# Optimization experiments

Measured on AMD Instinct MI355X. Metric: run time of the kernel, lower is better.

The kernel has to match this reference:

```python
import jax, jax.numpy as jnp
import numpy as np

B, L, DIM, HEADS = 2, 2048, 1536, 12
HD = DIM // HEADS  # 128
C = HD // 2        # 64 rotary pairs
EPS = 1e-6


def setup_inputs() -> dict:
    key = jax.random.key(0)
    ks = jax.random.split(key, 8)
    x = jax.random.normal(ks[0], (B, L, DIM), jnp.float32)
    # ragged grids: sample0 fills L, sample1 has 2*24*32 = 1536 valid tokens
    grid_sizes = jnp.array([[2, 32, 32], [2, 24, 32]], dtype=jnp.int32)
    seq_lens = jnp.array([2048, 1536], dtype=jnp.int32)
    # rope freqs table [1024, C] (cos/sin of pos * inv_freq)
    pos = jnp.arange(1024, dtype=jnp.float32)[:, None]
    inv = 1.0 / (10000.0 ** (jnp.arange(C, dtype=jnp.float32) / C))
    ang = pos * inv
    freqs_cos, freqs_sin = jnp.cos(ang), jnp.sin(ang)
    init = lambda k: jax.random.normal(k, (DIM, DIM), jnp.float32) / np.sqrt(DIM)
    return dict(
        x=x, seq_lens=seq_lens, grid_sizes=grid_sizes,
        freqs_cos=freqs_cos, freqs_sin=freqs_sin,
        Wq=init(ks[1]), bq=jnp.zeros((DIM,), jnp.float32),
        Wk=init(ks[2]), bk=jnp.zeros((DIM,), jnp.float32),
        Wv=init(ks[3]), bv=jnp.zeros((DIM,), jnp.float32),
        Wo=init(ks[4]), bo=jnp.zeros((DIM,), jnp.float32),
        gq=jnp.ones((DIM,), jnp.float32), gk=jnp.ones((DIM,), jnp.float32),
    )


def _rope_one(xb, grid, cos, sin):
    # xb: [L, n, d]; grid: (f, h, w); cos/sin: [1024, C]
    f, h, w = grid[0], grid[1], grid[2]
    c = cos.shape[1]
    c2 = c // 3
    c1 = c - 2 * c2  # freqs split [c1, c2, c2] over axes (f, h, w)
    p = jnp.arange(xb.shape[0])
    hw = h * w
    valid = p < f * hw
    fi = jnp.where(valid, p // hw, 0)
    hi = jnp.where(valid, (p // w) % h, 0)
    wi = jnp.where(valid, p % w, 0)
    cos_p = jnp.concatenate([cos[fi, :c1], cos[hi, c1:c1 + c2], cos[wi, c1 + c2:]], axis=-1)
    sin_p = jnp.concatenate([sin[fi, :c1], sin[hi, c1:c1 + c2], sin[wi, c1 + c2:]], axis=-1)
    # positions beyond seq_len pass through unrotated (identity rotation)
    cos_p = jnp.where(valid[:, None], cos_p, 1.0)[:, None, :]  # [L,1,C]
    sin_p = jnp.where(valid[:, None], sin_p, 0.0)[:, None, :]
    xr, xi = xb[..., 0::2], xb[..., 1::2]
    out_r = xr * cos_p - xi * sin_p
    out_i = xr * sin_p + xi * cos_p
    return jnp.stack([out_r, out_i], axis=-1).reshape(xb.shape)


_rope_apply = jax.vmap(_rope_one, in_axes=(0, 0, None, None))


def _rms(t, g):
    t32 = t.astype(jnp.float32)
    return (t32 * jax.lax.rsqrt(jnp.mean(t32 * t32, axis=-1, keepdims=True) + EPS) * g).astype(t.dtype)


def reference(x, seq_lens, grid_sizes, freqs_cos, freqs_sin,
              Wq, bq, Wk, bk, Wv, bv, Wo, bo, gq, gk):
    b, s = x.shape[:2]
    n, d = HEADS, HD
    q = _rms(x @ Wq + bq, gq).reshape(b, s, n, d)
    k = _rms(x @ Wk + bk, gk).reshape(b, s, n, d)
    v = (x @ Wv + bv).reshape(b, s, n, d)
    q = _rope_apply(q, grid_sizes, freqs_cos, freqs_sin)
    k = _rope_apply(k, grid_sizes, freqs_cos, freqs_sin)
    scale = 1.0 / np.sqrt(d).astype(np.float32)
    scores = jnp.einsum('bqnd,bknd->bnqk', q, k) * scale
    kmask = jnp.arange(s)[None, :] < seq_lens[:, None]  # [b, s] key validity
    scores = jnp.where(kmask[:, None, None, :], scores, jnp.float32(-1e9))
    attn = jax.nn.softmax(scores, axis=-1)
    out = jnp.einsum('bnqk,bknd->bqnd', attn, v).reshape(b, s, n * d)
    return out @ Wo + bo
```

## Files before the change

kernel.cpp:

```cpp
#include <hip/hip_runtime.h>
#include <hip/hip_bf16.h>

#define DIM   1536
#define HEADS 12
#define HD    128
#define LSEQ  2048
#define NB    2
#define NTOK  (NB*LSEQ)

using f32x4  = __attribute__((ext_vector_type(4))) float;
using f32x16 = __attribute__((ext_vector_type(16))) float;
using s16x8  = __attribute__((ext_vector_type(8))) short;
using u16x4  = __attribute__((ext_vector_type(4))) unsigned short;

__device__ __forceinline__ unsigned short f2bf(float f) {
  unsigned int u = __builtin_bit_cast(unsigned int, f);
  u += 0x7fffu + ((u >> 16) & 1u);
  return (unsigned short)(u >> 16);
}
__device__ __forceinline__ float bf2f(unsigned short u) {
  return __builtin_bit_cast(float, (unsigned int)u << 16);
}
__device__ __forceinline__ unsigned pk2(float a, float b) {
  unsigned r;
  asm("v_cvt_pk_bf16_f32 %0, %1, %2" : "=v"(r) : "v"(a), "v"(b));
  return r;
}
__device__ __forceinline__ unsigned long long pack4bf(float a, float b, float c, float d) {
  return (unsigned long long)f2bf(a) | ((unsigned long long)f2bf(b) << 16) |
         ((unsigned long long)f2bf(c) << 32) | ((unsigned long long)f2bf(d) << 48);
}
__device__ __forceinline__ void plswap(unsigned &x, unsigned &y) {
  asm volatile("v_permlane32_swap_b32 %0, %1" : "+v"(x), "+v"(y));
}
__device__ __forceinline__ void gload_lds16(const void* g, void* l) {
  __builtin_amdgcn_global_load_lds(
      (__attribute__((address_space(1))) void*)const_cast<void*>(g),
      (__attribute__((address_space(3))) void*)l,
      16, 0, 0);
}

__global__ __launch_bounds__(256) void cvt_x(const float* __restrict__ x,
                                             unsigned short* __restrict__ xb, int n) {
  int i = (blockIdx.x * 256 + threadIdx.x) * 4;
  int stride = gridDim.x * 256 * 4;
  for (; i < n; i += stride) {
    f32x4 v = *(const f32x4*)(x + i);
    u16x4 o;
    o[0] = f2bf(v[0]); o[1] = f2bf(v[1]); o[2] = f2bf(v[2]); o[3] = f2bf(v[3]);
    *(u16x4*)(xb + i) = o;
  }
}

__global__ __launch_bounds__(256) void wtrans(const float* W0, const float* W1,
                                              const float* W2, const float* W3,
                                              unsigned short* __restrict__ Wt) {
  const float* W = blockIdx.z == 0 ? W0 : blockIdx.z == 1 ? W1 : blockIdx.z == 2 ? W2 : W3;
  unsigned short* out = Wt + (size_t)blockIdx.z * DIM * DIM;
  const int n0 = blockIdx.x * 64, k0 = blockIdx.y * 64;
  __shared__ unsigned short t[64][68];
  const int tid = threadIdx.x;
#pragma unroll
  for (int i = 0; i < 16; i++) {
    int idx = tid + i * 256;
    int r = idx >> 6, c = idx & 63;
    t[r][c] = f2bf(W[(size_t)(k0 + r) * DIM + n0 + c]);
  }
  __syncthreads();
#pragma unroll
  for (int i = 0; i < 16; i++) {
    int idx = tid + i * 256;
    int r = idx >> 6, c = idx & 63;
    out[(size_t)(n0 + r) * DIM + k0 + c] = t[c][r];
  }
}

__global__ __launch_bounds__(256) void gemm_bt(
    const unsigned short* __restrict__ A, const unsigned short* __restrict__ Bt,
    void* __restrict__ Cv,
    const float* __restrict__ b0, const float* __restrict__ b1, const float* __restrict__ b2,
    int M, int N, int K, int biasMode, int outBf16) {
  __shared__ __align__(16) unsigned short As[128 * 64];
  __shared__ __align__(16) unsigned short Bs[128 * 64];
  const int tid = threadIdx.x;
  const int lane = tid & 63, w = tid >> 6;
  const int wr = w >> 1, wc = w & 1;
  const int l15 = lane & 15, g4 = lane >> 4;
  const int nwg = gridDim.x * gridDim.y;
  const int bidf = blockIdx.y * gridDim.x + blockIdx.x;
  const int cpx = nwg >> 3;
  const int sw = (bidf & 7) * cpx + (bidf >> 3);
  const int m0 = (sw / gridDim.x) * 128, n0 = (sw % gridDim.x) * 128;

  f32x4 acc[4][4];
#pragma unroll
  for (int i = 0; i < 4; i++)
#pragma unroll
    for (int j = 0; j < 4; j++) acc[i][j] = (f32x4){0.f, 0.f, 0.f, 0.f};

  for (int kt = 0; kt < K; kt += 64) {
    __syncthreads();
#pragma unroll
    for (int i = 0; i < 4; i++) {
      int c = tid + i * 256;
      int row = c >> 3, g = c & 7;
      int gs = g ^ (row & 7);
      gload_lds16(A + (size_t)(m0 + row) * K + kt + gs * 8, As + c * 8);
    }
#pragma unroll
    for (int i = 0; i < 4; i++) {
      int c = tid + i * 256;
      int row = c >> 3, g = c & 7;
      int gs = g ^ (row & 7);
      gload_lds16(Bt + (size_t)(n0 + row) * K + kt + gs * 8, Bs + c * 8);
    }
    __syncthreads();
#pragma unroll
    for (int kk = 0; kk < 2; kk++) {
      s16x8 af[4], bfr[4];
#pragma unroll
      for (int m = 0; m < 4; m++) {
        int row = wr * 64 + m * 16 + l15;
        int off = row * 128 + ((kk * 64 + g4 * 16) ^ ((row & 7) << 4));
        af[m] = *(const s16x8*)((const char*)As + off);
      }
#pragma unroll
      for (int n = 0; n < 4; n++) {
        int row = wc * 64 + n * 16 + l15;
        int off = row * 128 + ((kk * 64 + g4 * 16) ^ ((row & 7) << 4));
        bfr[n] = *(const s16x8*)((const char*)Bs + off);
      }
#pragma unroll
      for (int m = 0; m < 4; m++)
#pragma unroll
        for (int n = 0; n < 4; n++)
          acc[m][n] = __builtin_amdgcn_mfma_f32_16x16x32_bf16(af[m], bfr[n], acc[m][n], 0, 0, 0);
    }
  }
#pragma unroll
  for (int m = 0; m < 4; m++)
#pragma unroll
    for (int n = 0; n < 4; n++)
#pragma unroll
      for (int r = 0; r < 4; r++) {
        int grow = m0 + wr * 64 + m * 16 + g4 * 4 + r;
        int gcol = n0 + wc * 64 + n * 16 + l15;
        float bias = (biasMode == 1)
                         ? b0[gcol]
                         : (gcol < 1536 ? b0[gcol]
                                        : (gcol < 3072 ? b1[gcol - 1536] : b2[gcol - 3072]));
        float val = acc[m][n][r] + bias;
        if (outBf16) ((unsigned short*)Cv)[(size_t)grow * N + gcol] = f2bf(val);
        else         ((float*)Cv)[(size_t)grow * N + gcol] = val;
      }
}

__global__ __launch_bounds__(256) void rmsrope(
    const unsigned short* __restrict__ qkvb,
    const float* __restrict__ gq, const float* __restrict__ gk,
    const int* __restrict__ grid_sizes,
    const float* __restrict__ fcos, const float* __restrict__ fsin,
    unsigned short* __restrict__ qb, unsigned short* __restrict__ kb) {
  const int t = blockIdx.x;
  const int b = t >> 11, l = t & 2047;
  const int tid = threadIdx.x;
  __shared__ float qrow[1536], krow[1536];
  __shared__ float red[8];
  const unsigned short* rq = qkvb + (size_t)t * 4608;
  const unsigned short* rk = rq + 1536;
  float sq = 0.f, sk = 0.f;
  if (tid < 192) {
    s16x8 vq = *(const s16x8*)(rq + tid * 8);
    s16x8 vk = *(const s16x8*)(rk + tid * 8);
#pragma unroll
    for (int j = 0; j < 8; j++) {
      float a = bf2f((unsigned short)vq[j]); qrow[tid * 8 + j] = a; sq += a * a;
      float c = bf2f((unsigned short)vk[j]); krow[tid * 8 + j] = c; sk += c * c;
    }
  }
  for (int o = 32; o; o >>= 1) { sq += __shfl_down(sq, o); sk += __shfl_down(sk, o); }
  if ((tid & 63) == 0) { red[tid >> 6] = sq; red[4 + (tid >> 6)] = sk; }
  __syncthreads();
  const float rsq = rsqrtf((red[0] + red[1] + red[2] + red[3]) * (1.f / 1536.f) + 1e-6f);
  const float rsk = rsqrtf((red[4] + red[5] + red[6] + red[7]) * (1.f / 1536.f) + 1e-6f);
  const float QS = 0.08838834764831845f * 1.4426950408889634f;
  const int fg = grid_sizes[b * 3 + 0], hg = grid_sizes[b * 3 + 1], wg = grid_sizes[b * 3 + 2];
  const int hw = hg * wg;
  const bool valid = l < fg * hw;
  const int fi = valid ? l / hw : 0;
  const int hi = valid ? (l / wg) % hg : 0;
  const int wi = valid ? l % wg : 0;
  const size_t obase = (((size_t)b * HEADS) * LSEQ + l) * HD;
  for (int i = tid; i < HEADS * 64; i += 256) {
    int hd = i >> 6, j = i & 63;
    float c, s;
    if (valid) {
      int idx = j < 22 ? fi : (j < 43 ? hi : wi);
      c = fcos[idx * 64 + j]; s = fsin[idx * 64 + j];
    } else { c = 1.f; s = 0.f; }
    int col = hd * 128 + 2 * j;
    size_t o = obase + (size_t)hd * LSEQ * HD + 2 * j;
    float xr = qrow[col] * rsq * gq[col];
    float xi = qrow[col + 1] * rsq * gq[col + 1];
    float q0 = (xr * c - xi * s) * QS, q1 = (xr * s + xi * c) * QS;
    *(unsigned int*)(qb + o) = (unsigned int)f2bf(q0) | ((unsigned int)f2bf(q1) << 16);
    xr = krow[col] * rsk * gk[col];
    xi = krow[col + 1] * rsk * gk[col + 1];
    *(unsigned int*)(kb + o) =
        (unsigned int)f2bf(xr * c - xi * s) | ((unsigned int)f2bf(xr * s + xi * c) << 16);
  }
}

__global__ __launch_bounds__(256) void vtrans(const unsigned short* __restrict__ qkvb,
                                              unsigned short* __restrict__ vt) {
  const int lt = blockIdx.x, h = blockIdx.y, b = blockIdx.z;
  const int l0 = lt * 64;
  __shared__ unsigned short tile[64][130];
  const int tid = threadIdx.x;
#pragma unroll
  for (int i = 0; i < 4; i++) {
    int idx = tid + i * 256;
    int tk = idx >> 4, dc = (idx & 15) * 8;
    s16x8 v = *(const s16x8*)(qkvb + (size_t)(b * 2048 + l0 + tk) * 4608 + 3072 + h * 128 + dc);
#pragma unroll
    for (int j = 0; j < 8; j++) tile[tk][dc + j] = (unsigned short)v[j];
  }
  __syncthreads();
  const size_t ob = (((size_t)b * HEADS + h) * HD) * LSEQ + l0;
#pragma unroll
  for (int i = 0; i < 4; i++) {
    int idx = tid + i * 256;
    int d = idx >> 3, ck = (idx & 7) * 8;
    s16x8 o;
#pragma unroll
    for (int j = 0; j < 8; j++) o[j] = (short)tile[ck + j][d];
    *(s16x8*)(vt + ob + (size_t)d * LSEQ + ck) = o;
  }
}

__global__ __launch_bounds__(128) void flash(
    const unsigned short* __restrict__ qb, const unsigned short* __restrict__ kb,
    const unsigned short* __restrict__ vt, const int* __restrict__ seq_lens,
    unsigned short* __restrict__ ob) {
  const int orig = blockIdx.x + 32 * (blockIdx.y + 12 * blockIdx.z);
  const int wg = (orig & 7) * 96 + (orig >> 3);
  const int qt = wg & 31;
  const int hb = wg >> 5;
  const int hh = hb % 12, b = hb / 12;
  const int tid = threadIdx.x, lane = tid & 63, w = tid >> 6;
  const int l31 = lane & 31, hi = lane >> 5;
  __shared__ __align__(16) unsigned short Ks[2][32 * 128];
  __shared__ __align__(16) unsigned short Vs[2][128 * 32];
  const size_t bh = (size_t)b * HEADS + hh;
  const int q0 = qt * 64 + w * 32;

  s16x8 qf[8];
  {
    const unsigned short* qp = qb + (bh * LSEQ + q0 + l31) * HD + hi * 8;
#pragma unroll
    for (int s = 0; s < 8; s++) qf[s] = *(const s16x8*)(qp + s * 16);
  }
  const int ntile = seq_lens[b] >> 5;
  asm volatile("s_waitcnt vmcnt(0)" ::: "memory");

  f32x16 acc[4];
#pragma unroll
  for (int d = 0; d < 4; d++)
#pragma unroll
    for (int r = 0; r < 16; r++) acc[d][r] = 0.f;
  float mrow = -1e30f, ls = 0.f;

#define STAGE_K(T, BUF)                                                                \
  _Pragma("unroll") for (int i = 0; i < 4; i++) {                                      \
    int c = tid + i * 128, row = c >> 4, seg = c & 15, ss = seg ^ (row & 15);          \
    gload_lds16(kb + (bh * LSEQ + (T) * 32 + row) * HD + ss * 8, &Ks[BUF][0] + c * 8); \
  }
#define STAGE_V(T, BUF)                                                                \
  _Pragma("unroll") for (int i = 0; i < 4; i++) {                                      \
    int c = tid + i * 128, row = c >> 2, seg = c & 3, ss = seg ^ ((row >> 1) & 3);     \
    gload_lds16(vt + (bh * HD + row) * LSEQ + (T) * 32 + ss * 8, &Vs[BUF][0] + c * 8); \
  }

  STAGE_K(0, 0); STAGE_V(0, 0);
  STAGE_K(1, 1); STAGE_V(1, 1);

  for (int kt = 0; kt < ntile; kt++) {
    const int cur = kt & 1;
    asm volatile("s_waitcnt vmcnt(8)" ::: "memory");
    __builtin_amdgcn_s_barrier();
    __builtin_amdgcn_sched_barrier(0);
    f32x16 st0;
#pragma unroll
    for (int r = 0; r < 16; r++) st0[r] = 0.f;
    const char* ksb = (const char*)&Ks[cur][0];
    __builtin_amdgcn_s_setprio(1);
#pragma unroll
    for (int s = 0; s < 8; s++) {
      int g = 2 * s + hi;
      s16x8 kf = *(const s16x8*)(ksb + l31 * 256 + ((g ^ (l31 & 15)) << 4));
      st0 = __builtin_amdgcn_mfma_f32_32x32x16_bf16(kf, qf[s], st0, 0, 0, 0);
    }
    __builtin_amdgcn_s_setprio(0);
    f32x16 mt;
#pragma unroll
    for (int r = 0; r < 16; r++) mt[r] = st0[r];
#pragma unroll
    for (int off = 8; off; off >>= 1)
#pragma unroll
      for (int r = 0; r < off; r++) mt[r] = fmaxf(mt[r], mt[r + off]);
    float mx = fmaxf(mt[0], __shfl_xor(mt[0], 32));
    const bool grow = mx > mrow + 8.0f;
    const float alpha = grow ? exp2f(mrow - mx) : 1.f;
    if (grow) mrow = mx;
#pragma unroll
    for (int r = 0; r < 16; r++) st0[r] = exp2f(st0[r] - mrow);
    f32x16 sm;
#pragma unroll
    for (int r = 0; r < 16; r++) sm[r] = st0[r];
#pragma unroll
    for (int off = 8; off; off >>= 1)
#pragma unroll
      for (int r = 0; r < off; r++) sm[r] += sm[r + off];
    ls = ls * alpha + (sm[0] + __shfl_xor(sm[0], 32));
    if (__any((int)grow)) {
#pragma unroll
      for (int d = 0; d < 4; d++)
#pragma unroll
        for (int r = 0; r < 16; r++) acc[d][r] *= alpha;
    }
    union U { unsigned u[4]; s16x8 v; } pa0, pa1;
    {
      unsigned c0 = pk2(st0[0], st0[1]),  c1 = pk2(st0[2], st0[3]);
      unsigned c2 = pk2(st0[4], st0[5]),  c3 = pk2(st0[6], st0[7]);
      unsigned c4 = pk2(st0[8], st0[9]),  c5 = pk2(st0[10], st0[11]);
      unsigned c6 = pk2(st0[12], st0[13]), c7 = pk2(st0[14], st0[15]);
      plswap(c0, c2); plswap(c1, c3); plswap(c4, c6); plswap(c5, c7);
      pa0.u[0] = c0; pa0.u[1] = c1; pa0.u[2] = c2; pa0.u[3] = c3;
      pa1.u[0] = c4; pa1.u[1] = c5; pa1.u[2] = c6; pa1.u[3] = c7;
    }
    const char* vsb = (const char*)&Vs[cur][0];
    __builtin_amdgcn_s_setprio(1);
#pragma unroll
    for (int slot = 0; slot < 2; slot++) {
      s16x8 pb = slot == 0 ? pa0.v : pa1.v;
      int g = 2 * slot + hi;
#pragma unroll
      for (int d = 0; d < 4; d++) {
        int row = d * 32 + l31;
        s16x8 vf = *(const s16x8*)(vsb + row * 64 + ((g ^ ((row >> 1) & 3)) << 4));
        acc[d] = __builtin_amdgcn_mfma_f32_32x32x16_bf16(vf, pb, acc[d], 0, 0, 0);
      }
    }
    __builtin_amdgcn_s_setprio(0);
    __builtin_amdgcn_s_barrier();
    __builtin_amdgcn_sched_barrier(0);
    {
      int knext = (kt + 2 < ntile) ? kt + 2 : kt;
      STAGE_K(knext, cur); STAGE_V(knext, cur);
    }
  }
  asm volatile("s_waitcnt vmcnt(0)" ::: "memory");
#undef STAGE_K
#undef STAGE_V
  const float invl = 1.f / ls;
  unsigned short* op = ob + (size_t)(b * LSEQ + q0 + l31) * DIM + hh * HD + hi * 4;
#pragma unroll
  for (int d = 0; d < 4; d++)
#pragma unroll
    for (int j = 0; j < 4; j++) {
      unsigned long long pk = pack4bf(acc[d][4 * j] * invl, acc[d][4 * j + 1] * invl,
                                      acc[d][4 * j + 2] * invl, acc[d][4 * j + 3] * invl);
      *(unsigned long long*)(op + d * 32 + 8 * j) = pk;
    }
}

extern "C" void kernel_launch(void* const* d_in, const int* in_sizes, int n_in,
                              void* d_out, int out_size, void* d_ws, size_t ws_size,
                              hipStream_t stream) {
  const float* x    = (const float*)d_in[0];
  const int*   seq  = (const int*)d_in[1];
  const int*   grids= (const int*)d_in[2];
  const float* fcos = (const float*)d_in[3];
  const float* fsin = (const float*)d_in[4];
  const float* Wq   = (const float*)d_in[5];
  const float* bq   = (const float*)d_in[6];
  const float* Wk   = (const float*)d_in[7];
  const float* bk   = (const float*)d_in[8];
  const float* Wv   = (const float*)d_in[9];
  const float* bv   = (const float*)d_in[10];
  const float* Wo   = (const float*)d_in[11];
  const float* bo   = (const float*)d_in[12];
  const float* gq   = (const float*)d_in[13];
  const float* gk   = (const float*)d_in[14];

  char* ws = (char*)d_ws;
  unsigned short* xb   = (unsigned short*)(ws);
  unsigned short* Wt   = (unsigned short*)(ws + 12582912);
  unsigned short* qkvb = (unsigned short*)(ws + 31457280);
  unsigned short* qbb  = (unsigned short*)(ws + 69206016);
  unsigned short* kbb  = (unsigned short*)(ws + 81788928);
  unsigned short* vt   = (unsigned short*)d_out;
  unsigned short* obb  = xb;
  float* out = (float*)d_out;

  cvt_x<<<1024, 256, 0, stream>>>(x, xb, NTOK * DIM);
  wtrans<<<dim3(24, 24, 4), 256, 0, stream>>>(Wq, Wk, Wv, Wo, Wt);
  gemm_bt<<<dim3(36, 32), 256, 0, stream>>>(xb, Wt, qkvb, bq, bk, bv, NTOK, 3 * DIM, DIM, 0, 1);
  rmsrope<<<NTOK, 256, 0, stream>>>(qkvb, gq, gk, grids, fcos, fsin, qbb, kbb);
  vtrans<<<dim3(32, 12, 2), 256, 0, stream>>>(qkvb, vt);
  flash<<<dim3(32, 12, 2), 128, 0, stream>>>(qbb, kbb, vt, seq, obb);
  gemm_bt<<<dim3(12, 32), 256, 0, stream>>>(obb, Wt + (size_t)3 * DIM * DIM, out,
                                            bo, bo, bo, NTOK, DIM, DIM, 1, 0);
}
```

Measured before the change: 246.9 us.

## Split attention KV range in two and merge partial results

The flash kernel now splits each (batch, head, query-tile) work item into two halves of the key range. This doubles the grid size so more waves are in flight on the GPU. Each half writes its unnormalized bf16 partial output plus its row max and row sum to workspace. A new merge kernel rescales and combines the two halves into the normalized output. The cost is extra global traffic, a second kernel launch, and bf16 rounding of the unnormalized partial accumulators.

```diff
diff --git a/kernel.cpp b/kernel.cpp
--- a/kernel.cpp
+++ b/kernel.cpp
@@ -241,12 +241,14 @@
 __global__ __launch_bounds__(128) void flash(
     const unsigned short* __restrict__ qb, const unsigned short* __restrict__ kb,
     const unsigned short* __restrict__ vt, const int* __restrict__ seq_lens,
-    unsigned short* __restrict__ ob) {
+    unsigned short* __restrict__ pO, float* __restrict__ pls, float* __restrict__ pm) {
   const int orig = blockIdx.x + 32 * (blockIdx.y + 12 * blockIdx.z);
-  const int wg = (orig & 7) * 96 + (orig >> 3);
+  const int wg = (orig & 7) * 192 + (orig >> 3);
   const int qt = wg & 31;
-  const int hb = wg >> 5;
-  const int hh = hb % 12, b = hb / 12;
+  const int r5 = wg >> 5;
+  const int hh = r5 % 12;
+  const int z2 = r5 / 12;
+  const int b = z2 >> 1, half = z2 & 1;
   const int tid = threadIdx.x, lane = tid & 63, w = tid >> 6;
   const int l31 = lane & 31, hi = lane >> 5;
   __shared__ __align__(16) unsigned short Ks[2][32 * 128];
@@ -261,6 +263,9 @@
     for (int s = 0; s < 8; s++) qf[s] = *(const s16x8*)(qp + s * 16);
   }
   const int ntile = seq_lens[b] >> 5;
+  const int htiles = ntile >> 1;
+  const int k0t = half * htiles;
+  const int kend = k0t + htiles;
   asm volatile("s_waitcnt vmcnt(0)" ::: "memory");
 
   f32x16 acc[4];
@@ -281,10 +286,10 @@
     gload_lds16(vt + (bh * HD + row) * LSEQ + (T) * 32 + ss * 8, &Vs[BUF][0] + c * 8); \
   }
 
-  STAGE_K(0, 0); STAGE_V(0, 0);
-  STAGE_K(1, 1); STAGE_V(1, 1);
-
-  for (int kt = 0; kt < ntile; kt++) {
+  STAGE_K(k0t, 0); STAGE_V(k0t, 0);
+  STAGE_K(k0t + 1, 1); STAGE_V(k0t + 1, 1);
+
+  for (int kt = k0t; kt < kend; kt++) {
     const int cur = kt & 1;
     asm volatile("s_waitcnt vmcnt(8)" ::: "memory");
     __builtin_amdgcn_s_barrier();
@@ -355,23 +360,53 @@
     __builtin_amdgcn_s_barrier();
     __builtin_amdgcn_sched_barrier(0);
     {
-      int knext = (kt + 2 < ntile) ? kt + 2 : kt;
+      int knext = (kt + 2 < kend) ? kt + 2 : kt;
       STAGE_K(knext, cur); STAGE_V(knext, cur);
     }
   }
   asm volatile("s_waitcnt vmcnt(0)" ::: "memory");
 #undef STAGE_K
 #undef STAGE_V
-  const float invl = 1.f / ls;
-  unsigned short* op = ob + (size_t)(b * LSEQ + q0 + l31) * DIM + hh * HD + hi * 4;
+  const int p = ((b * 12 + hh) * 32 + qt) * 2 + half;
+  const int ql = w * 32 + l31;
+  unsigned short* pop = pO + ((size_t)p * 64 + ql) * 128 + hi * 4;
 #pragma unroll
   for (int d = 0; d < 4; d++)
 #pragma unroll
     for (int j = 0; j < 4; j++) {
-      unsigned long long pk = pack4bf(acc[d][4 * j] * invl, acc[d][4 * j + 1] * invl,
-                                      acc[d][4 * j + 2] * invl, acc[d][4 * j + 3] * invl);
-      *(unsigned long long*)(op + d * 32 + 8 * j) = pk;
-    }
+      unsigned long long pk = pack4bf(acc[d][4 * j], acc[d][4 * j + 1],
+                                      acc[d][4 * j + 2], acc[d][4 * j + 3]);
+      *(unsigned long long*)(pop + d * 32 + 8 * j) = pk;
+    }
+  if (hi == 0) {
+    pls[(size_t)p * 64 + ql] = ls;
+    pm[(size_t)p * 64 + ql] = mrow;
+  }
+}
+
+__global__ __launch_bounds__(256) void merge(
+    const unsigned short* __restrict__ pO, const float* __restrict__ pls,
+    const float* __restrict__ pm, unsigned short* __restrict__ ob) {
+  const int qt = blockIdx.x, h = blockIdx.y, b = blockIdx.z;
+  const int p0 = ((b * 12 + h) * 32 + qt) * 2;
+  const int tid = threadIdx.x;
+#pragma unroll
+  for (int i = tid; i < 1024; i += 256) {
+    int q = i >> 4, c = (i & 15) * 8;
+    float m0 = pm[(size_t)p0 * 64 + q],  m1 = pm[(size_t)(p0 + 1) * 64 + q];
+    float l0 = pls[(size_t)p0 * 64 + q], l1 = pls[(size_t)(p0 + 1) * 64 + q];
+    float m = fmaxf(m0, m1);
+    float a0 = exp2f(m0 - m), a1 = exp2f(m1 - m);
+    float inv = 1.f / (a0 * l0 + a1 * l1);
+    a0 *= inv; a1 *= inv;
+    s16x8 o0 = *(const s16x8*)(pO + ((size_t)p0 * 64 + q) * 128 + c);
+    s16x8 o1 = *(const s16x8*)(pO + ((size_t)(p0 + 1) * 64 + q) * 128 + c);
+    s16x8 o;
+#pragma unroll
+    for (int j = 0; j < 8; j++)
+      o[j] = (short)f2bf(bf2f((unsigned short)o0[j]) * a0 + bf2f((unsigned short)o1[j]) * a1);
+    *(s16x8*)(ob + ((size_t)(b * LSEQ) + qt * 64 + q) * DIM + h * HD + c) = o;
+  }
 }
 
 extern "C" void kernel_launch(void* const* d_in, const int* in_sizes, int n_in,
@@ -399,6 +434,9 @@
   unsigned short* qkvb = (unsigned short*)(ws + 31457280);
   unsigned short* qbb  = (unsigned short*)(ws + 69206016);
   unsigned short* kbb  = (unsigned short*)(ws + 81788928);
+  unsigned short* pO   = (unsigned short*)(ws + 31457280);
+  float*          pls  = (float*)(ws + 31457280 + 25165824);
+  float*          pm   = (float*)(ws + 31457280 + 25165824 + 393216);
   unsigned short* vt   = (unsigned short*)d_out;
   unsigned short* obb  = xb;
   float* out = (float*)d_out;
@@ -408,7 +446,8 @@
   gemm_bt<<<dim3(36, 32), 256, 0, stream>>>(xb, Wt, qkvb, bq, bk, bv, NTOK, 3 * DIM, DIM, 0, 1);
   rmsrope<<<NTOK, 256, 0, stream>>>(qkvb, gq, gk, grids, fcos, fsin, qbb, kbb);
   vtrans<<<dim3(32, 12, 2), 256, 0, stream>>>(qkvb, vt);
-  flash<<<dim3(32, 12, 2), 128, 0, stream>>>(qbb, kbb, vt, seq, obb);
+  flash<<<dim3(32, 12, 4), 128, 0, stream>>>(qbb, kbb, vt, seq, pO, pls, pm);
+  merge<<<dim3(32, 12, 2), 256, 0, stream>>>(pO, pls, pm, obb);
   gemm_bt<<<dim3(12, 32), 256, 0, stream>>>(obb, Wt + (size_t)3 * DIM * DIM, out,
                                             bo, bo, bo, NTOK, DIM, DIM, 1, 0);
 }
```

Measured after the change: 261.8 us. 6.0% more time.
